# Kernel tuning notes

Hardware: AMD Instinct MI355X
Metric: run time of the kernel (lower is better)

## Reference

```python
import jax, jax.numpy as jnp
import numpy as np

GROUPS = 8
EPS = 1e-3  # Keras GroupNormalization default epsilon


def group_norm(x, gamma, beta):
    b, h, w, c = x.shape
    xr = x.reshape(b, h, w, GROUPS, c // GROUPS)
    mean = jnp.mean(xr, axis=(1, 2, 4), keepdims=True)
    var = jnp.var(xr, axis=(1, 2, 4), keepdims=True)
    xn = ((xr - mean) * jax.lax.rsqrt(var + EPS)).reshape(b, h, w, c)
    return xn * gamma + beta


def setup_inputs() -> dict:
    key = jax.random.key(0)
    ks = jax.random.split(key, 6)
    B, H, W, C = 4, 64, 64, 256
    std = C ** -0.5
    return {
        "x": jax.random.normal(ks[0], (B, H, W, C), dtype=jnp.float32),
        "gamma": jnp.ones((C,), jnp.float32),
        "beta": jnp.zeros((C,), jnp.float32),
        "wq": jax.random.normal(ks[1], (C, C), jnp.float32) * std,
        "bq": jnp.zeros((C,), jnp.float32),
        "wk": jax.random.normal(ks[2], (C, C), jnp.float32) * std,
        "bk": jnp.zeros((C,), jnp.float32),
        "wv": jax.random.normal(ks[3], (C, C), jnp.float32) * std,
        "bv": jnp.zeros((C,), jnp.float32),
        "wp": jax.random.normal(ks[4], (C, C), jnp.float32) * std,
        "bp": jnp.zeros((C,), jnp.float32),
    }


def reference(x, gamma, beta, wq, bq, wk, bk, wv, bv, wp, bp):
    b, h, w, c = x.shape
    scale = jnp.asarray(c, x.dtype) ** -0.5
    xn = group_norm(x, gamma, beta)
    # 1x1 convs are per-pixel dense layers
    q = (xn @ wq + bq).reshape(b, h * w, c)
    k = (xn @ wk + bk).reshape(b, h * w, c)
    v = (xn @ wv + bv).reshape(b, h * w, c)
    scores = jnp.einsum('bic,bjc->bij', q, k) * scale  # [b, N, N]
    attn = jax.nn.softmax(scores, axis=-1)
    out = jnp.einsum('bij,bjc->bic', attn, v).reshape(b, h, w, c)
    return x + (out @ wp + bp)
```

## Files before the change

kernel.cpp:

```cpp
#include <hip/hip_runtime.h>

#define N_TOK 4096
#define C_DIM 256
#define BATCH 4
#define M_ROWS (BATCH * N_TOK)
#define GN_CNT 131072.0f
#define JSPLIT 4

typedef __attribute__((ext_vector_type(4))) float f32x4;
typedef __attribute__((ext_vector_type(16))) float f32x16;
typedef __attribute__((ext_vector_type(8))) short s16x8;
typedef __attribute__((ext_vector_type(4))) unsigned short u16x4;
typedef __attribute__((ext_vector_type(4))) unsigned int u32x4;

static __device__ __forceinline__ unsigned short f2bf(float f) {
  unsigned int u = __builtin_bit_cast(unsigned int, f);
  u += 0x7fff + ((u >> 16) & 1);
  return (unsigned short)(u >> 16);
}
static __device__ __forceinline__ float bf2f(unsigned short h) {
  unsigned int u = ((unsigned int)h) << 16;
  return __builtin_bit_cast(float, u);
}

static __device__ __forceinline__ void gload_lds16(const void* g, void* l) {
  __builtin_amdgcn_global_load_lds(
      (__attribute__((address_space(1))) void*)(unsigned long long)(const char*)g,
      (__attribute__((address_space(3))) void*)l, 16, 0, 0);
}

__global__ __launch_bounds__(256) void prep(const float* __restrict__ x,
                                            const float* __restrict__ wq,
                                            const float* __restrict__ wk,
                                            const float* __restrict__ wv,
                                            const float* __restrict__ wp,
                                            float* __restrict__ partials,
                                            unsigned short* __restrict__ wT) {
  int tid = threadIdx.x;
  if (blockIdx.x < 512) {
    int bg = blockIdx.x >> 4, chunk = blockIdx.x & 15;
    int b = bg >> 3, g = bg & 7;
    const f32x4* x4 = (const f32x4*)x;
    float s1 = 0.f, s2 = 0.f;
#pragma unroll
    for (int it = 0; it < 8; ++it) {
      int idx = it * 256 + tid;
      int nl = idx >> 3, cq = idx & 7;
      f32x4 v = x4[(b * N_TOK + chunk * 256 + nl) * 64 + g * 8 + cq];
      s1 += v[0] + v[1] + v[2] + v[3];
      s2 += v[0] * v[0] + v[1] * v[1] + v[2] * v[2] + v[3] * v[3];
    }
    for (int m = 1; m < 64; m <<= 1) {
      s1 += __shfl_xor(s1, m, 64);
      s2 += __shfl_xor(s2, m, 64);
    }
    __shared__ float r1[4], r2[4];
    int wave = tid >> 6, lane = tid & 63;
    if (lane == 0) { r1[wave] = s1; r2[wave] = s2; }
    __syncthreads();
    if (tid == 0) {
      int slot = (bg * 16 + chunk) * 2;
      partials[slot]     = r1[0] + r1[1] + r1[2] + r1[3];
      partials[slot + 1] = r2[0] + r2[1] + r2[2] + r2[3];
    }
  } else {
    int rem = blockIdx.x - 512;
    int z = rem >> 6, t = rem & 63;
    int k0 = (t >> 3) * 32, n0 = (t & 7) * 32;
    const float* const srcs[4] = {wq, wk, wv, wp};
    const float* w = srcs[z];
    unsigned short* o = wT + z * 65536;
    __shared__ float tt[32][33];
    int tx = tid & 31, ty = tid >> 5;
#pragma unroll
    for (int ky = 0; ky < 32; ky += 8)
      tt[ty + ky][tx] = w[(k0 + ty + ky) * C_DIM + n0 + tx];
    __syncthreads();
#pragma unroll
    for (int ky = 0; ky < 32; ky += 8)
      o[(n0 + ty + ky) * C_DIM + k0 + tx] = f2bf(tt[tx][ty + ky]);
  }
}

__global__ __launch_bounds__(256, 2) void qkv_gemm(const float* __restrict__ x,
                                                   const unsigned short* __restrict__ wT,
                                                   const float* __restrict__ partials,
                                                   const float* __restrict__ gamma,
                                                   const float* __restrict__ beta,
                                                   const float* __restrict__ bq,
                                                   const float* __restrict__ bk,
                                                   const float* __restrict__ bv,
                                                   unsigned short* __restrict__ qo,
                                                   unsigned short* __restrict__ ko,
                                                   unsigned short* __restrict__ vo) {
  int tid = threadIdx.x;
  int wave = tid >> 6, lane = tid & 63, n32 = lane & 31, half = lane >> 5;
  int row0 = blockIdx.x * 128 + wave * 32;
  int c0 = blockIdx.y * 128;
  int row = row0 + n32;
  int batch = blockIdx.x >> 5;
  __shared__ __align__(16) unsigned short Wt[32768];
  __shared__ float mean_s[8], rstd_s[8];

#pragma unroll
  for (int ii = 0; ii < 32; ++ii) {
    int u = ii * 256 + tid;
    int n = u >> 5, ku = u & 31;
    gload_lds16(wT + (size_t)(c0 + n) * C_DIM + ((ku ^ (n & 7)) * 8), Wt + u * 8);
  }
  if (tid < 8) {
    const float* p = partials + (batch * 8 + tid) * 32;
    float s1 = 0.f, s2 = 0.f;
#pragma unroll
    for (int c = 0; c < 16; ++c) { s1 += p[2 * c]; s2 += p[2 * c + 1]; }
    float inv = 1.f / GN_CNT;
    float m = s1 * inv, v = s2 * inv - m * m;
    mean_s[tid] = m;
    rstd_s[tid] = rsqrtf(v + 1e-3f);
  }
  __syncthreads();

  float mean[8], rstd[8];
#pragma unroll
  for (int g = 0; g < 8; ++g) { mean[g] = mean_s[g]; rstd[g] = rstd_s[g]; }
  s16x8 af[16];
#pragma unroll
  for (int ks = 0; ks < 16; ++ks) {
    int cb = ks * 16 + half * 8;
    const f32x4* xp = (const f32x4*)(x + (size_t)row * C_DIM + cb);
    f32x4 v0 = xp[0], v1 = xp[1];
    const f32x4* g4 = (const f32x4*)(gamma + cb);
    const f32x4* b4 = (const f32x4*)(beta + cb);
    f32x4 ga0 = g4[0], ga1 = g4[1], be0 = b4[0], be1 = b4[1];
    int g = (2 * ks + half) >> 2;
    float m = mean[g], rs = rstd[g];
    s16x8 o;
#pragma unroll
    for (int j = 0; j < 4; ++j) {
      o[j]     = (short)f2bf((v0[j] - m) * rs * ga0[j] + be0[j]);
      o[4 + j] = (short)f2bf((v1[j] - m) * rs * ga1[j] + be1[j]);
    }
    af[ks] = o;
  }

  for (int w = 0; w < 3; ++w) {
    if (w > 0) {
      __syncthreads();
#pragma unroll
      for (int ii = 0; ii < 32; ++ii) {
        int u = ii * 256 + tid;
        int n = u >> 5, ku = u & 31;
        gload_lds16(wT + (size_t)w * 65536 + (size_t)(c0 + n) * C_DIM + ((ku ^ (n & 7)) * 8),
                    Wt + u * 8);
      }
      __syncthreads();
    }
    const float* bias = (w == 0) ? bq : (w == 1) ? bk : bv;
    unsigned short* outp = (w == 0) ? qo : (w == 1) ? ko : vo;
    float scale = (w == 0) ? 0.0625f : 1.f;
#pragma unroll
    for (int ct = 0; ct < 4; ++ct) {
      int nl = ct * 32 + n32;
      f32x16 acc = (f32x16)(bias[c0 + nl]);
#pragma unroll
      for (int ks = 0; ks < 16; ++ks) {
        s16x8 wf = *(const s16x8*)(Wt + nl * C_DIM + (((2 * ks + half) ^ (nl & 7)) * 8));
        acc = __builtin_amdgcn_mfma_f32_32x32x16_bf16(af[ks], wf, acc, 0, 0, 0);
      }
#pragma unroll
      for (int r = 0; r < 16; ++r) {
        int rr = (r & 3) + 8 * (r >> 2) + 4 * half;
        outp[(size_t)(row0 + rr) * C_DIM + c0 + nl] = f2bf(acc[r] * scale);
      }
    }
  }
}

__global__ __launch_bounds__(256) void vtrans(const unsigned short* __restrict__ v,
                                              unsigned short* __restrict__ vT) {
  __shared__ unsigned short t[32][33];
  int n0 = blockIdx.x * 32, c0 = blockIdx.y * 32, b = blockIdx.z;
  int tx = threadIdx.x, ty = threadIdx.y;
#pragma unroll
  for (int ky = 0; ky < 32; ky += 8)
    t[ty + ky][tx] = v[(b * N_TOK + n0 + ty + ky) * C_DIM + c0 + tx];
  __syncthreads();
#pragma unroll
  for (int ky = 0; ky < 32; ky += 8)
    vT[(b * C_DIM + c0 + ty + ky) * N_TOK + n0 + tx] = t[tx][ty + ky];
}

__global__ __launch_bounds__(256, 2) void attn_part(const unsigned short* __restrict__ q,
                                                    const unsigned short* __restrict__ k,
                                                    const unsigned short* __restrict__ vT,
                                                    unsigned short* __restrict__ op0,
                                                    unsigned short* __restrict__ op1,
                                                    unsigned short* __restrict__ op2,
                                                    unsigned short* __restrict__ op3,
                                                    float* __restrict__ lbuf) {
  int tid = threadIdx.x;
  int wave = tid >> 6, lane = tid & 63;
  int n32 = lane & 31, half = lane >> 5;
  int i = blockIdx.x;
  int batch = (i >> 1) & 3;
  int slot = ((i >> 3) << 1) | (i & 1);
  int qb = slot & 31, chunk = slot >> 5;
  int qrow0 = batch * N_TOK + qb * 128 + wave * 32;
  const unsigned short* kb = k + (size_t)batch * N_TOK * C_DIM;
  const unsigned short* vb = vT + (size_t)batch * C_DIM * N_TOK;
  unsigned short* op = (chunk == 0) ? op0 : (chunk == 1) ? op1 : (chunk == 2) ? op2 : op3;

  __shared__ __align__(16) unsigned short Kt[2][8192];
  __shared__ __align__(16) unsigned short Vt[2][8192];

  const unsigned short* qp = q + (size_t)(qrow0 + n32) * C_DIM;
  s16x8 qf[16];
#pragma unroll
  for (int ks = 0; ks < 16; ++ks)
    qf[ks] = *(const s16x8*)(qp + ks * 16 + half * 8);

  f32x16 Oa[8];
#pragma unroll
  for (int ct = 0; ct < 8; ++ct) Oa[ct] = (f32x16)(0.f);
  float ls = 0.f;
  int swz = n32 & 7;

  {
    int jbase = chunk * 1024;
#pragma unroll
    for (int ii = 0; ii < 4; ++ii) {
      int u = ii * 256 + tid;
      int tok = u >> 5, un = u & 31;
      gload_lds16(kb + (size_t)(jbase + tok) * C_DIM + ((un ^ (tok & 7)) * 8), &Kt[0][u * 8]);
    }
#pragma unroll
    for (int ii = 0; ii < 4; ++ii) {
      gload_lds16(vb + (size_t)tid * N_TOK + jbase + ii * 8, &Vt[0][(ii * 256 + tid) * 8]);
    }
  }

  int cur = 0;
  for (int jt = 0; jt < 32; ++jt) {
    __syncthreads();
    if (jt < 31) {
      int jbase = chunk * 1024 + (jt + 1) * 32;
      int nxt = cur ^ 1;
#pragma unroll
      for (int ii = 0; ii < 4; ++ii) {
        int u = ii * 256 + tid;
        int tok = u >> 5, un = u & 31;
        gload_lds16(kb + (size_t)(jbase + tok) * C_DIM + ((un ^ (tok & 7)) * 8), &Kt[nxt][u * 8]);
      }
#pragma unroll
      for (int ii = 0; ii < 4; ++ii) {
        gload_lds16(vb + (size_t)tid * N_TOK + jbase + ii * 8, &Vt[nxt][(ii * 256 + tid) * 8]);
      }
    }
    const unsigned short* KT = Kt[cur];
    const unsigned short* VT = Vt[cur];

    f32x16 sc = (f32x16)(0.f);
#pragma unroll
    for (int ks = 0; ks < 16; ++ks) {
      s16x8 kf = *(const s16x8*)(KT + n32 * 256 + (((ks * 2 + half) ^ swz) * 8));
      sc = __builtin_amdgcn_mfma_f32_32x32x16_bf16(kf, qf[ks], sc, 0, 0, 0);
    }
    unsigned D[8];
#pragma unroll
    for (int t = 0; t < 8; ++t) {
      float pa = exp2f(fmaf(sc[2 * t],     1.44269504f, -11.54156032f));
      float pb = exp2f(fmaf(sc[2 * t + 1], 1.44269504f, -11.54156032f));
      ls += pa + pb;
      D[t] = (__builtin_bit_cast(unsigned, pa) >> 16) |
             (__builtin_bit_cast(unsigned, pb) & 0xFFFF0000u);
    }
    unsigned E[8];
#pragma unroll
    for (int t = 0; t < 8; ++t) E[t] = __shfl_xor(D[t], 32);
    u32x4 w0 = {half ? E[2] : D[0], half ? E[3] : D[1],
                half ? D[2] : E[0], half ? D[3] : E[1]};
    u32x4 w1 = {half ? E[6] : D[4], half ? E[7] : D[5],
                half ? D[6] : E[4], half ? D[7] : E[5]};
    s16x8 pf0 = __builtin_bit_cast(s16x8, w0);
    s16x8 pf1 = __builtin_bit_cast(s16x8, w1);
#pragma unroll
    for (int ct = 0; ct < 8; ++ct) {
      int ch = ct * 32 + n32;
      s16x8 vf0 = *(const s16x8*)(VT + (half * 256 + ch) * 8);
      s16x8 vf1 = *(const s16x8*)(VT + ((2 + half) * 256 + ch) * 8);
      Oa[ct] = __builtin_amdgcn_mfma_f32_32x32x16_bf16(pf0, vf0, Oa[ct], 0, 0, 0);
      Oa[ct] = __builtin_amdgcn_mfma_f32_32x32x16_bf16(pf1, vf1, Oa[ct], 0, 0, 0);
    }
    cur ^= 1;
  }
#pragma unroll
  for (int ct = 0; ct < 8; ++ct)
#pragma unroll
    for (int r = 0; r < 16; ++r) {
      int row = (r & 3) + 8 * (r >> 2) + 4 * half;
      op[(size_t)(qrow0 + row) * C_DIM + ct * 32 + n32] = f2bf(Oa[ct][r]);
    }
  float tot = ls + __shfl_xor(ls, 32);
  if (half == 0) lbuf[chunk * M_ROWS + qrow0 + n32] = tot;
}

__global__ __launch_bounds__(256, 2) void proj_gemm(const unsigned short* __restrict__ p0,
                                                    const unsigned short* __restrict__ p1,
                                                    const unsigned short* __restrict__ p2,
                                                    const unsigned short* __restrict__ p3,
                                                    const float* __restrict__ lbuf,
                                                    const unsigned short* __restrict__ wt,
                                                    const float* __restrict__ bp,
                                                    const float* __restrict__ x,
                                                    float* __restrict__ out) {
  int tid = threadIdx.x;
  int wave = tid >> 6, lane = tid & 63, n32 = lane & 31, half = lane >> 5;
  int row0 = blockIdx.x * 128 + wave * 32;
  int c0 = blockIdx.y * 128;
  __shared__ __align__(16) unsigned short Wt[32768];

#pragma unroll
  for (int ii = 0; ii < 32; ++ii) {
    int u = ii * 256 + tid;
    int n = u >> 5, ku = u & 31;
    gload_lds16(wt + (size_t)(c0 + n) * C_DIM + ((ku ^ (n & 7)) * 8), Wt + u * 8);
  }

  int row = row0 + n32;
  float linv = 1.f / (lbuf[row] + lbuf[M_ROWS + row] +
                      lbuf[2 * M_ROWS + row] + lbuf[3 * M_ROWS + row]);
  s16x8 af[16];
#pragma unroll
  for (int ks = 0; ks < 16; ++ks) {
    size_t off = (size_t)row * C_DIM + ks * 16 + half * 8;
    s16x8 a0 = *(const s16x8*)(p0 + off);
    s16x8 a1 = *(const s16x8*)(p1 + off);
    s16x8 a2 = *(const s16x8*)(p2 + off);
    s16x8 a3 = *(const s16x8*)(p3 + off);
    s16x8 o;
#pragma unroll
    for (int j = 0; j < 8; ++j) {
      float f = bf2f((unsigned short)a0[j]) + bf2f((unsigned short)a1[j]) +
                bf2f((unsigned short)a2[j]) + bf2f((unsigned short)a3[j]);
      o[j] = (short)f2bf(f * linv);
    }
    af[ks] = o;
  }
  __syncthreads();

#pragma unroll
  for (int ct = 0; ct < 4; ++ct) {
    int nl = ct * 32 + n32;
    f32x16 acc = (f32x16)(bp[c0 + nl]);
#pragma unroll
    for (int ks = 0; ks < 16; ++ks) {
      s16x8 wf = *(const s16x8*)(Wt + nl * C_DIM + (((2 * ks + half) ^ (nl & 7)) * 8));
      acc = __builtin_amdgcn_mfma_f32_32x32x16_bf16(af[ks], wf, acc, 0, 0, 0);
    }
#pragma unroll
    for (int r = 0; r < 16; ++r) {
      int rr = (r & 3) + 8 * (r >> 2) + 4 * half;
      size_t idx = (size_t)(row0 + rr) * C_DIM + c0 + nl;
      out[idx] = acc[r] + x[idx];
    }
  }
}

extern "C" void kernel_launch(void* const* d_in, const int* in_sizes, int n_in,
                              void* d_out, int out_size, void* d_ws, size_t ws_size,
                              hipStream_t stream) {
  const float* x     = (const float*)d_in[0];
  const float* gamma = (const float*)d_in[1];
  const float* beta  = (const float*)d_in[2];
  const float* wq    = (const float*)d_in[3];
  const float* bq    = (const float*)d_in[4];
  const float* wk    = (const float*)d_in[5];
  const float* bk    = (const float*)d_in[6];
  const float* wv    = (const float*)d_in[7];
  const float* bv    = (const float*)d_in[8];
  const float* wp    = (const float*)d_in[9];
  const float* bp    = (const float*)d_in[10];
  float* out = (float*)d_out;

  char* ws = (char*)d_ws;
  const size_t MC = (size_t)M_ROWS * C_DIM;
  float* partials      = (float*)ws;
  unsigned short* wT   = (unsigned short*)(ws + 4096);
  unsigned short* qb   = wT + 4 * 65536;
  unsigned short* kbuf = qb + MC;
  unsigned short* vb   = kbuf + MC;
  unsigned short* vTb  = vb + MC;
  unsigned short* pl0  = vTb + MC;
  unsigned short* pl2  = pl0 + MC;
  unsigned short* pl3  = pl2 + MC;
  float* lbuf          = (float*)(pl3 + MC);
  unsigned short* pl1  = vb;

  prep<<<768, 256, 0, stream>>>(x, wq, wk, wv, wp, partials, wT);
  qkv_gemm<<<dim3(128, 2), 256, 0, stream>>>(x, wT, partials, gamma, beta,
                                             bq, bk, bv, qb, kbuf, vb);
  vtrans<<<dim3(128, 8, 4), dim3(32, 8), 0, stream>>>(vb, vTb);
  attn_part<<<512, 256, 0, stream>>>(qb, kbuf, vTb, pl0, pl1, pl2, pl3, lbuf);
  proj_gemm<<<dim3(128, 2), 256, 0, stream>>>(pl0, pl1, pl2, pl3, lbuf,
                                              wT + 3 * 65536, bp, x, out);
}
```

Measured before the change: 219.5 us.

## Software-pipeline attention loop: overlap softmax of tile j with PV of tile j-1

Restructures the attention inner loop so the exp/pack of the current score tile is interleaved with the P·V MFMAs of the previous tile, using a triple-buffered V LDS ring and a double-buffered K ring. K staging layout changes from an XOR-swizzled row layout to a ks-major layout, and s_setprio raises wave priority around the MFMA section. This aims to hide exp/shuffle latency behind matrix work, at the cost of extra LDS (now 80KB per block, which may limit the intended 2 blocks/CU) and more registers.

```diff
diff --git a/kernel.cpp b/kernel.cpp
--- a/kernel.cpp
+++ b/kernel.cpp
@@ -190,6 +190,36 @@
     vT[(b * C_DIM + c0 + ty + ky) * N_TOK + n0 + tx] = t[tx][ty + ky];
 }
 
+static __device__ __forceinline__ void stage_K(unsigned short* dst,
+                                               const unsigned short* kb,
+                                               int jbase, int tid) {
+#pragma unroll
+  for (int ii = 0; ii < 4; ++ii) {
+    int u = ii * 256 + tid;
+    int ksu = u >> 6, tok = (u >> 1) & 31, hf = u & 1;
+    gload_lds16(kb + (size_t)(jbase + tok) * C_DIM + ksu * 16 + hf * 8, dst + u * 8);
+  }
+}
+static __device__ __forceinline__ void stage_V(unsigned short* dst,
+                                               const unsigned short* vb,
+                                               int jbase, int tid) {
+#pragma unroll
+  for (int ii = 0; ii < 4; ++ii)
+    gload_lds16(vb + (size_t)tid * N_TOK + jbase + ii * 8, dst + (ii * 256 + tid) * 8);
+}
+
+static __device__ __forceinline__ f32x16 qk_compute(const unsigned short* KT,
+                                                    const s16x8* qf,
+                                                    int n32, int half) {
+  f32x16 sc = (f32x16)(0.f);
+#pragma unroll
+  for (int ks = 0; ks < 16; ++ks) {
+    s16x8 kf = *(const s16x8*)(KT + ks * 512 + (n32 * 2 + half) * 8);
+    sc = __builtin_amdgcn_mfma_f32_32x32x16_bf16(kf, qf[ks], sc, 0, 0, 0);
+  }
+  return sc;
+}
+
 __global__ __launch_bounds__(256, 2) void attn_part(const unsigned short* __restrict__ q,
                                                     const unsigned short* __restrict__ k,
                                                     const unsigned short* __restrict__ vT,
@@ -210,8 +240,12 @@
   const unsigned short* vb = vT + (size_t)batch * C_DIM * N_TOK;
   unsigned short* op = (chunk == 0) ? op0 : (chunk == 1) ? op1 : (chunk == 2) ? op2 : op3;
 
-  __shared__ __align__(16) unsigned short Kt[2][8192];
-  __shared__ __align__(16) unsigned short Vt[2][8192];
+  __shared__ __align__(16) unsigned short K_lds[2][8192];
+  __shared__ __align__(16) unsigned short V_lds[3][8192];
+
+  int jbase0 = chunk * 1024;
+  stage_K(K_lds[0], kb, jbase0, tid);
+  stage_V(V_lds[0], vb, jbase0, tid);
 
   const unsigned short* qp = q + (size_t)(qrow0 + n32) * C_DIM;
   s16x8 qf[16];
@@ -223,49 +257,16 @@
 #pragma unroll
   for (int ct = 0; ct < 8; ++ct) Oa[ct] = (f32x16)(0.f);
   float ls = 0.f;
-  int swz = n32 & 7;
-
+
+  __syncthreads();
+
+  stage_K(K_lds[1], kb, jbase0 + 32, tid);
+  stage_V(V_lds[1], vb, jbase0 + 32, tid);
+
+  s16x8 pf0p, pf1p;
   {
-    int jbase = chunk * 1024;
-#pragma unroll
-    for (int ii = 0; ii < 4; ++ii) {
-      int u = ii * 256 + tid;
-      int tok = u >> 5, un = u & 31;
-      gload_lds16(kb + (size_t)(jbase + tok) * C_DIM + ((un ^ (tok & 7)) * 8), &Kt[0][u * 8]);
-    }
-#pragma unroll
-    for (int ii = 0; ii < 4; ++ii) {
-      gload_lds16(vb + (size_t)tid * N_TOK + jbase + ii * 8, &Vt[0][(ii * 256 + tid) * 8]);
-    }
-  }
-
-  int cur = 0;
-  for (int jt = 0; jt < 32; ++jt) {
-    __syncthreads();
-    if (jt < 31) {
-      int jbase = chunk * 1024 + (jt + 1) * 32;
-      int nxt = cur ^ 1;
-#pragma unroll
-      for (int ii = 0; ii < 4; ++ii) {
-        int u = ii * 256 + tid;
-        int tok = u >> 5, un = u & 31;
-        gload_lds16(kb + (size_t)(jbase + tok) * C_DIM + ((un ^ (tok & 7)) * 8), &Kt[nxt][u * 8]);
-      }
-#pragma unroll
-      for (int ii = 0; ii < 4; ++ii) {
-        gload_lds16(vb + (size_t)tid * N_TOK + jbase + ii * 8, &Vt[nxt][(ii * 256 + tid) * 8]);
-      }
-    }
-    const unsigned short* KT = Kt[cur];
-    const unsigned short* VT = Vt[cur];
-
-    f32x16 sc = (f32x16)(0.f);
-#pragma unroll
-    for (int ks = 0; ks < 16; ++ks) {
-      s16x8 kf = *(const s16x8*)(KT + n32 * 256 + (((ks * 2 + half) ^ swz) * 8));
-      sc = __builtin_amdgcn_mfma_f32_32x32x16_bf16(kf, qf[ks], sc, 0, 0, 0);
-    }
-    unsigned D[8];
+    f32x16 sc = qk_compute(K_lds[0], qf, n32, half);
+    unsigned D[8], E[8];
 #pragma unroll
     for (int t = 0; t < 8; ++t) {
       float pa = exp2f(fmaf(sc[2 * t],     1.44269504f, -11.54156032f));
@@ -273,26 +274,67 @@
       ls += pa + pb;
       D[t] = (__builtin_bit_cast(unsigned, pa) >> 16) |
              (__builtin_bit_cast(unsigned, pb) & 0xFFFF0000u);
-    }
-    unsigned E[8];
-#pragma unroll
-    for (int t = 0; t < 8; ++t) E[t] = __shfl_xor(D[t], 32);
+      E[t] = __shfl_xor(D[t], 32);
+    }
     u32x4 w0 = {half ? E[2] : D[0], half ? E[3] : D[1],
                 half ? D[2] : E[0], half ? D[3] : E[1]};
     u32x4 w1 = {half ? E[6] : D[4], half ? E[7] : D[5],
                 half ? D[6] : E[4], half ? D[7] : E[5]};
-    s16x8 pf0 = __builtin_bit_cast(s16x8, w0);
-    s16x8 pf1 = __builtin_bit_cast(s16x8, w1);
-#pragma unroll
-    for (int ct = 0; ct < 8; ++ct) {
-      int ch = ct * 32 + n32;
-      s16x8 vf0 = *(const s16x8*)(VT + (half * 256 + ch) * 8);
-      s16x8 vf1 = *(const s16x8*)(VT + ((2 + half) * 256 + ch) * 8);
-      Oa[ct] = __builtin_amdgcn_mfma_f32_32x32x16_bf16(pf0, vf0, Oa[ct], 0, 0, 0);
-      Oa[ct] = __builtin_amdgcn_mfma_f32_32x32x16_bf16(pf1, vf1, Oa[ct], 0, 0, 0);
-    }
-    cur ^= 1;
-  }
+    pf0p = __builtin_bit_cast(s16x8, w0);
+    pf1p = __builtin_bit_cast(s16x8, w1);
+  }
+
+  int vr_i = 0, vw_i = 2;
+  for (int jt = 1; jt < 32; ++jt) {
+    __syncthreads();
+    if (jt < 31) {
+      int jb2 = jbase0 + (jt + 1) * 32;
+      stage_K(K_lds[(jt + 1) & 1], kb, jb2, tid);
+      stage_V(V_lds[vw_i], vb, jb2, tid);
+    }
+    __builtin_amdgcn_s_setprio(1);
+    f32x16 sc = qk_compute(K_lds[jt & 1], qf, n32, half);
+
+    const unsigned short* VR = V_lds[vr_i];
+    unsigned D[8], E[8];
+#pragma unroll
+    for (int t = 0; t < 8; ++t) {
+      float pa = exp2f(fmaf(sc[2 * t],     1.44269504f, -11.54156032f));
+      float pb = exp2f(fmaf(sc[2 * t + 1], 1.44269504f, -11.54156032f));
+      ls += pa + pb;
+      D[t] = (__builtin_bit_cast(unsigned, pa) >> 16) |
+             (__builtin_bit_cast(unsigned, pb) & 0xFFFF0000u);
+      E[t] = __shfl_xor(D[t], 32);
+      int ch = t * 32 + n32;
+      s16x8 vf0 = *(const s16x8*)(VR + (half * 256 + ch) * 8);
+      s16x8 vf1 = *(const s16x8*)(VR + ((2 + half) * 256 + ch) * 8);
+      Oa[t] = __builtin_amdgcn_mfma_f32_32x32x16_bf16(pf0p, vf0, Oa[t], 0, 0, 0);
+      Oa[t] = __builtin_amdgcn_mfma_f32_32x32x16_bf16(pf1p, vf1, Oa[t], 0, 0, 0);
+    }
+    __builtin_amdgcn_s_setprio(0);
+
+    u32x4 w0 = {half ? E[2] : D[0], half ? E[3] : D[1],
+                half ? D[2] : E[0], half ? D[3] : E[1]};
+    u32x4 w1 = {half ? E[6] : D[4], half ? E[7] : D[5],
+                half ? D[6] : E[4], half ? D[7] : E[5]};
+    pf0p = __builtin_bit_cast(s16x8, w0);
+    pf1p = __builtin_bit_cast(s16x8, w1);
+    vr_i = (vr_i == 2) ? 0 : vr_i + 1;
+    vw_i = (vw_i == 2) ? 0 : vw_i + 1;
+  }
+
+  {
+    const unsigned short* VR = V_lds[vr_i];
+#pragma unroll
+    for (int t = 0; t < 8; ++t) {
+      int ch = t * 32 + n32;
+      s16x8 vf0 = *(const s16x8*)(VR + (half * 256 + ch) * 8);
+      s16x8 vf1 = *(const s16x8*)(VR + ((2 + half) * 256 + ch) * 8);
+      Oa[t] = __builtin_amdgcn_mfma_f32_32x32x16_bf16(pf0p, vf0, Oa[t], 0, 0, 0);
+      Oa[t] = __builtin_amdgcn_mfma_f32_32x32x16_bf16(pf1p, vf1, Oa[t], 0, 0, 0);
+    }
+  }
+
 #pragma unroll
   for (int ct = 0; ct < 8; ++ct)
 #pragma unroll
```

Measured after the change: 222.3 us. No clear change (+1.3%).
